# Kernel optimization log

Measured on AMD Instinct MI355X. Metric: run time of the kernel, lower is better.

## Reference

```python
import jax, jax.numpy as jnp
import numpy as np

B, S, D, H = 4, 1024, 1024, 16
HD = D // H


def setup_inputs() -> dict:
    key = jax.random.key(0)
    ks = jax.random.split(key, 12)
    s = 1.0 / np.sqrt(D)
    inp = {
        'q': jax.random.normal(ks[0], (B, S, D), jnp.float32),
        'k': jax.random.normal(ks[1], (B, S, D), jnp.float32),
        'v': jax.random.normal(ks[2], (B, S, D), jnp.float32),
        'mask': jnp.broadcast_to(jnp.tril(jnp.ones((S, S), jnp.int32)), (B, S, S)),
        'Wq': jax.random.uniform(ks[3], (D, D), jnp.float32, -s, s),
        'bq': jax.random.uniform(ks[4], (D,), jnp.float32, -s, s),
        'Wk': jax.random.uniform(ks[5], (D, D), jnp.float32, -s, s),
        'bk': jax.random.uniform(ks[6], (D,), jnp.float32, -s, s),
        'Wv': jax.random.uniform(ks[7], (D, D), jnp.float32, -s, s),
        'bv': jax.random.uniform(ks[8], (D,), jnp.float32, -s, s),
        'Wo': jax.random.uniform(ks[9], (D, D), jnp.float32, -s, s),
        'bo': jax.random.uniform(ks[10], (D,), jnp.float32, -s, s),
    }
    return inp


def _split_heads(x):
    # [B,S,D] -> [B,H,S,HD]
    b, s, d = x.shape
    return x.reshape(b, s, H, HD).transpose(0, 2, 1, 3)


def reference(q, k, v, mask, Wq, bq, Wk, bk, Wv, bv, Wo, bo):
    # Linear projections (torch Linear: x @ W.T + b) followed by relu
    qh = jax.nn.relu(q @ Wq.T + bq)
    kh = jax.nn.relu(k @ Wk.T + bk)
    vh = jax.nn.relu(v @ Wv.T + bv)
    qh, kh, vh = _split_heads(qh), _split_heads(kh), _split_heads(vh)
    scores = jnp.einsum('bhqd,bhkd->bhqk', qh, kh) / jnp.sqrt(jnp.float32(HD))
    scores = jnp.where(mask[:, None, :, :] == 0, jnp.float32(-1e9), scores)
    attn = jax.nn.softmax(scores, axis=-1)
    y = jnp.einsum('bhqk,bhkd->bhqd', attn, vh)
    y = y.transpose(0, 2, 1, 3).reshape(B, S, D)  # merge heads
    return jax.nn.relu(y @ Wo.T + bo)
```

## Files before the change

kernel.cpp:

```cpp
#include <hip/hip_runtime.h>


using f16    = _Float16;
using f16x4  = __attribute__((ext_vector_type(4))) _Float16;
using f16x8  = __attribute__((ext_vector_type(8))) _Float16;
using f32x4  = __attribute__((ext_vector_type(4))) float;
using f32x16 = __attribute__((ext_vector_type(16))) float;

static constexpr int S = 1024, Dm = 1024, NH = 16, HD = 64;

#if __has_builtin(__builtin_amdgcn_mfma_f32_32x32x16_f16)
#define USE_G32 1
#define MFMA32(ACC, A_, B_) \
    (ACC) = __builtin_amdgcn_mfma_f32_32x32x16_f16((A_), (B_), (ACC), 0, 0, 0)
#else
#define USE_G32 0
#endif

#if __has_builtin(__builtin_amdgcn_mfma_f32_16x16x32_f16) && \
    __has_builtin(__builtin_amdgcn_mfma_f32_16x16x16f16)
#define USE_A16 1
#define MFMA16K32(ACC, A_, B_) \
    (ACC) = __builtin_amdgcn_mfma_f32_16x16x32_f16((A_), (B_), (ACC), 0, 0, 0)
#define MFMA16(ACC, A_, B_) \
    (ACC) = __builtin_amdgcn_mfma_f32_16x16x16f16((A_), (B_), (ACC), 0, 0, 0)
#else
#define USE_A16 0
#endif

#define LO4(v) __builtin_shufflevector((v), (v), 0, 1, 2, 3)
#define HI4(v) __builtin_shufflevector((v), (v), 4, 5, 6, 7)

__device__ __forceinline__ f16x4 cvt4(float4 a) {
    f16x4 r; r[0] = (f16)a.x; r[1] = (f16)a.y; r[2] = (f16)a.z; r[3] = (f16)a.w;
    return r;
}

__device__ __forceinline__ int pcol64(int k) {
#if USE_A16
    return ((k >> 3) & 3) * 16 + ((k >> 5) << 3) + (k & 7);
#else
    return ((k >> 2) & 3) * 16 + ((k >> 4) << 2) + (k & 3);
#endif
}

__device__ __forceinline__ int swz(int row, int col) {
    return (col & ~31) | ((((col >> 3) ^ (row >> 1)) & 3) << 3) | (col & 7);
}

__device__ __forceinline__ void store_out(void* out, int mode, int m, int n, float v) {
    const int b_ = m >> 10, s_ = m & 1023, h_ = n >> 6, hd_ = n & 63;
    const size_t idx = (mode == 0)
        ? (((size_t)(b_ * NH + h_) * S + s_) * HD + pcol64(hd_))
        : (((size_t)(b_ * NH + h_) * HD + hd_) * S + s_);
    ((f16*)out)[idx] = (f16)v;
}

#if __has_builtin(__builtin_amdgcn_global_load_lds)
#define HAS_GLL 1
#else
#define HAS_GLL 0
#endif

__device__ __forceinline__ void gll16(const void* g, void* l) {
#if HAS_GLL
    __builtin_amdgcn_global_load_lds(
        (const __attribute__((address_space(1))) void*)g,
        (__attribute__((address_space(3))) void*)l, 16, 0, 0);
#else
    *(uint4*)l = *(const uint4*)g;
#endif
}

__global__ __launch_bounds__(256)
void cvt_w(const float* __restrict__ s0, const float* __restrict__ s1,
           const float* __restrict__ s2, f16* __restrict__ dst)
{
    const int z = blockIdx.y;
    const float* src = (z == 0) ? s0 : (z == 1) ? s1 : s2;
    const int e = blockIdx.x * 256 + threadIdx.x;
    const int n = e >> 8;
    const int k = (e & 255) * 4;
    const float4 v = *(const float4*)(src + (size_t)n * Dm + k);
    *(f16x4*)(dst + (size_t)z * Dm * Dm + (size_t)n * Dm + swz(n, k)) = cvt4(v);
}

__global__ __launch_bounds__(512, 6)
void gemm_qkv(const float* __restrict__ q, const float* __restrict__ k,
              const float* __restrict__ v, const f16* __restrict__ wqkv,
              const float* __restrict__ bq, const float* __restrict__ bk,
              const float* __restrict__ bv,
              f16* __restrict__ qh, f16* __restrict__ kh, f16* __restrict__ vt)
{
    const int z = blockIdx.z;
    const float* A = (z == 0) ? q : (z == 1) ? k : v;
    const float* bias = (z == 0) ? bq : (z == 1) ? bk : bv;
    f16* out = (z == 0) ? qh : (z == 1) ? kh : vt;
    const int mode = (z == 2) ? 1 : 0;
    const f16* Wf = wqkv + (size_t)z * Dm * Dm;

    const int tid = threadIdx.x;
    const int bm = blockIdx.x, bn = blockIdx.y;
#if USE_G32
    __shared__ alignas(16) float As[2][128][32];
    __shared__ alignas(16) f16   Ws[2][128][32];

    const int lane = tid & 63, wave = tid >> 6;
    const int l31 = lane & 31, kh2 = lane >> 5;
    const int wm = wave & 3, wn = wave >> 2;

    const int arow = tid >> 3;
    const int aslotD = tid & 7;
    const int aslotS = aslotD ^ (arow & 7);
    const float* Asrc0 = A + (size_t)(bm * 128 + arow) * Dm + aslotS * 4;
    const int wrow = tid >> 2, wcol = (tid & 3) * 8;
    const f16* Wsrc0 = Wf + (size_t)(bn * 128 + wrow) * Dm + wcol;

    auto dma = [&](int k0, int buf) {
        gll16(Asrc0 + k0,                      &As[buf][arow][aslotD * 4]);
        gll16(Asrc0 + (size_t)64 * Dm + k0,    &As[buf][64 + arow][aslotD * 4]);
        gll16(Wsrc0 + k0,                      &Ws[buf][wrow][wcol]);
    };

    auto afrag = [&](int buf, int r, int s) -> f16x8 {
        const int p = s * 4 + kh2 * 2, r7 = r & 7;
        const f32x4 lo = *(const f32x4*)&As[buf][r][(p ^ r7) * 4];
        const f32x4 hi = *(const f32x4*)&As[buf][r][((p + 1) ^ r7) * 4];
        f16x8 f;
        f[0] = (f16)lo[0]; f[1] = (f16)lo[1]; f[2] = (f16)lo[2]; f[3] = (f16)lo[3];
        f[4] = (f16)hi[0]; f[5] = (f16)hi[1]; f[6] = (f16)hi[2]; f[7] = (f16)hi[3];
        return f;
    };
    auto wfrag = [&](int buf, int r, int s) -> f16x8 {
        const int sl = s * 2 + kh2;
        return *(const f16x8*)&Ws[buf][r][((sl ^ (r >> 1)) & 3) * 8];
    };

    f32x16 acc[2] = {};
    auto kslice = [&](int buf, int s) {
        const f16x8 af  = afrag(buf, wm * 32 + l31, s);
        const f16x8 bf0 = wfrag(buf, wn * 64 + l31, s);
        const f16x8 bf1 = wfrag(buf, wn * 64 + 32 + l31, s);
        MFMA32(acc[0], af, bf0);
        MFMA32(acc[1], af, bf1);
    };

    constexpr int NIT = Dm / 32;
    dma(0, 0);
    for (int t = 0; t < NIT; ++t) {
        const int cur = t & 1;
        __syncthreads();
        if (t + 1 < NIT) dma((t + 1) * 32, cur ^ 1);
        kslice(cur, 0);
        kslice(cur, 1);
    }

#pragma unroll
    for (int j = 0; j < 2; ++j) {
        const int col = bn * 128 + wn * 64 + j * 32 + l31;
        const float bb = bias[col];
#pragma unroll
        for (int blk = 0; blk < 4; ++blk) {
            const int row0 = bm * 128 + wm * 32 + 8 * blk + 4 * kh2;
            if (mode == 1) {
                const int b_ = row0 >> 10, s_ = row0 & 1023;
                const int h_ = col >> 6, hd_ = col & 63;
                f16x4 vv;
#pragma unroll
                for (int r = 0; r < 4; ++r)
                    vv[r] = (f16)fmaxf(acc[j][blk * 4 + r] + bb, 0.0f);
                *(f16x4*)&out[((size_t)(b_ * NH + h_) * HD + hd_) * S + s_] = vv;
            } else {
#pragma unroll
                for (int r = 0; r < 4; ++r)
                    store_out(out, mode, row0 + r, col,
                              fmaxf(acc[j][blk * 4 + r] + bb, 0.0f));
            }
        }
    }
#else
    for (int i = tid; i < 128 * 128; i += 512) {
        const int m = bm * 128 + (i >> 7);
        const int n = bn * 128 + (i & 127);
        float acc = 0.0f;
        for (int k2 = 0; k2 < Dm; ++k2)
            acc = fmaf(A[(size_t)m * Dm + k2], (float)Wf[(size_t)n * Dm + swz(n, k2)], acc);
        store_out(out, mode, m, n, fmaxf(acc + bias[n], 0.0f));
    }
#endif
}

__global__ __launch_bounds__(256, 6)
void gemm_out(const f16* __restrict__ y, const float* __restrict__ wo,
              const float* __restrict__ bo, float* __restrict__ out)
{
    const int tid = threadIdx.x;
    const int bm = blockIdx.x, bn = blockIdx.y;
#if USE_G32
    __shared__ alignas(16) f16   As[2][64][32];
    __shared__ alignas(16) float Wsf[2][64][32];

    const int lane = tid & 63, wave = tid >> 6;
    const int l31 = lane & 31, kh2 = lane >> 5;
    const int wm = wave & 1, wn = wave >> 1;

    const int drow = tid >> 2, dcol = (tid & 3) * 8;
    const f16* Asrc = y + (size_t)(bm * 64 + drow) * Dm + dcol;
    const int wrow = tid >> 3;
    const int wslotD = tid & 7;
    const int wslotS = wslotD ^ (wrow & 7);
    const float* Wsrc0 = wo + (size_t)(bn * 64 + wrow) * Dm + wslotS * 4;

    auto dma = [&](int k0, int buf) {
        gll16(Asrc + k0, &As[buf][drow][dcol]);
        gll16(Wsrc0 + k0,                   &Wsf[buf][wrow][wslotD * 4]);
        gll16(Wsrc0 + (size_t)32 * Dm + k0, &Wsf[buf][32 + wrow][wslotD * 4]);
    };
    auto yfrag = [&](int buf, int r, int s) -> f16x8 {
        const int sl = s * 2 + kh2;
        return *(const f16x8*)&As[buf][r][((sl ^ (r >> 1)) & 3) * 8];
    };
    auto wfrag32 = [&](int buf, int r, int s) -> f16x8 {
        const int p = s * 4 + kh2 * 2, r7 = r & 7;
        const f32x4 lo = *(const f32x4*)&Wsf[buf][r][(p ^ r7) * 4];
        const f32x4 hi = *(const f32x4*)&Wsf[buf][r][((p + 1) ^ r7) * 4];
        f16x8 f;
        f[0] = (f16)lo[0]; f[1] = (f16)lo[1]; f[2] = (f16)lo[2]; f[3] = (f16)lo[3];
        f[4] = (f16)hi[0]; f[5] = (f16)hi[1]; f[6] = (f16)hi[2]; f[7] = (f16)hi[3];
        return f;
    };

    f32x16 acc = {};
    constexpr int NIT = Dm / 32;
    dma(0, 0);
    for (int t = 0; t < NIT; ++t) {
        const int cur = t & 1;
        __syncthreads();
        if (t + 1 < NIT) dma((t + 1) * 32, cur ^ 1);
#pragma unroll
        for (int s = 0; s < 2; ++s) {
            const f16x8 af = yfrag(cur, wm * 32 + l31, s);
            const f16x8 bf = wfrag32(cur, wn * 32 + l31, s);
            MFMA32(acc, af, bf);
        }
    }

    const int col = bn * 64 + wn * 32 + l31;
    const float bb = bo[col];
#pragma unroll
    for (int blk = 0; blk < 4; ++blk) {
        const int row0 = bm * 64 + wm * 32 + 8 * blk + 4 * kh2;
#pragma unroll
        for (int r = 0; r < 4; ++r)
            out[(size_t)(row0 + r) * Dm + col] = fmaxf(acc[blk * 4 + r] + bb, 0.0f);
    }
#else
    for (int i = tid; i < 64 * 64; i += 256) {
        const int m = bm * 64 + (i >> 6);
        const int n = bn * 64 + (i & 63);
        float acc = 0.0f;
        for (int k2 = 0; k2 < Dm; ++k2)
            acc = fmaf((float)y[(size_t)m * Dm + swz(m, k2)],
                       wo[(size_t)n * Dm + k2], acc);
        out[(size_t)m * Dm + n] = fmaxf(acc + bo[n], 0.0f);
    }
#endif
}

__global__ __launch_bounds__(512, 6)
void attn_fwd(const f16* __restrict__ qh, const f16* __restrict__ kh,
              const f16* __restrict__ vt, f16* __restrict__ y)
{
    const int bz = blockIdx.x;
    const int qt = bz & 7;
    const int h  = (bz >> 3) & 15;
    const int b  = bz >> 7;
    const size_t head = (size_t)(b * NH + h) * S * HD;

#if USE_A16
    __shared__ alignas(16) f16 Ks[2][64][72];
    __shared__ alignas(16) f16 Vs[2][64][72];

    const int tid  = threadIdx.x;
    const int wave = tid >> 6;
    const int lane = tid & 63;
    const int l15  = lane & 15;
    const int quad = lane >> 4;
    const int sr   = tid >> 3;
    const int t8   = tid & 7;

    const f16* Qrow = qh + head + (size_t)(qt * 128 + wave * 16 + l15) * HD;
    const f16* Kp   = kh + head;
    const f16* Vp   = vt + head;

    f16x8 aq[2];
    {
        const uint4 q0 = *(const uint4*)(Qrow + quad * 16);
        const uint4 q1 = *(const uint4*)(Qrow + quad * 16 + 8);
        aq[0] = *(f16x8*)&q0;
        aq[1] = *(f16x8*)&q1;
    }

    const int qg = qt * 128 + wave * 16 + l15;
    float m_i = -1e30f, l_i = 0.0f;
    f32x4 acc_o[4] = {};

    const int vc0 = 16 * ((2 * t8) & 3) + 4 * (t8 >> 1);
    const int vc1 = 16 * ((2 * t8 + 1) & 3) + 4 * (t8 >> 1);

    uint4 pk, pv;
    auto pref = [&](int kt) {
        pk = *(const uint4*)(Kp + (size_t)(kt * 64 + sr) * HD + t8 * 8);
        pv = *(const uint4*)(Vp + (size_t)sr * S + kt * 64 + t8 * 8);
    };

    const int ktmax = 2 * qt + 1;
    pref(0);
    for (int kt = 0; kt <= ktmax; ++kt) {
        const int cur = kt & 1;
        *(uint4*)&Ks[cur][sr][t8 * 8] = pk;
        {
            f16x8 pv8 = *(f16x8*)&pv;
            *(f16x4*)&Vs[cur][sr][vc0] = LO4(pv8);
            *(f16x4*)&Vs[cur][sr][vc1] = HI4(pv8);
        }
        __syncthreads();
        if (kt < ktmax) pref(kt + 1);

        f32x4 accs[4] = {};
#pragma unroll
        for (int t = 0; t < 4; ++t) {
            const f16x8 k8a = *(const f16x8*)&Ks[cur][t * 16 + l15][quad * 16];
            const f16x8 k8b = *(const f16x8*)&Ks[cur][t * 16 + l15][quad * 16 + 8];
            MFMA16K32(accs[t], k8a, aq[0]);
            MFMA16K32(accs[t], k8b, aq[1]);
        }

        const int key0 = kt * 64 + quad * 4;
#pragma unroll
        for (int t = 0; t < 4; ++t)
#pragma unroll
            for (int r = 0; r < 4; ++r) {
                float sv = accs[t][r] * 0.125f;
                if (key0 + t * 16 + r > qg) sv = -1e9f;
                accs[t][r] = sv;
            }

        float mx = accs[0][0];
#pragma unroll
        for (int t = 0; t < 4; ++t)
#pragma unroll
            for (int r = 0; r < 4; ++r) mx = fmaxf(mx, accs[t][r]);
        mx = fmaxf(mx, __shfl_xor(mx, 16, 64));
        mx = fmaxf(mx, __shfl_xor(mx, 32, 64));
        const float mnew = fmaxf(m_i, mx);
        float sm = 0.0f;
#pragma unroll
        for (int t = 0; t < 4; ++t)
#pragma unroll
            for (int r = 0; r < 4; ++r) {
                const float e = __expf(accs[t][r] - mnew);
                accs[t][r] = e;
                sm += e;
            }
        sm += __shfl_xor(sm, 16, 64);
        sm += __shfl_xor(sm, 32, 64);
        const float alpha = __expf(m_i - mnew);
        l_i = l_i * alpha + sm;
        m_i = mnew;

        f16x4 ap[4];
#pragma unroll
        for (int c = 0; c < 4; ++c) {
            f16x4 v;
#pragma unroll
            for (int j = 0; j < 4; ++j) v[j] = (f16)accs[c][j];
            ap[c] = v;
        }

        float ar[4];
#pragma unroll
        for (int r = 0; r < 4; ++r) ar[r] = __shfl(alpha, quad * 4 + r, 64);
#pragma unroll
        for (int t2 = 0; t2 < 4; ++t2)
#pragma unroll
            for (int r = 0; r < 4; ++r) acc_o[t2][r] *= ar[r];
#pragma unroll
        for (int t2 = 0; t2 < 4; ++t2) {
            const f16x8 v8a = *(const f16x8*)&Vs[cur][t2 * 16 + l15][quad * 16];
            const f16x8 v8b = *(const f16x8*)&Vs[cur][t2 * 16 + l15][quad * 16 + 8];
            MFMA16(acc_o[t2], ap[0], LO4(v8a));
            MFMA16(acc_o[t2], ap[1], HI4(v8a));
            MFMA16(acc_o[t2], ap[2], LO4(v8b));
            MFMA16(acc_o[t2], ap[3], HI4(v8b));
        }
    }

    float lr[4];
#pragma unroll
    for (int r = 0; r < 4; ++r) lr[r] = __shfl(l_i, quad * 4 + r, 64);
#pragma unroll
    for (int t2 = 0; t2 < 4; ++t2)
#pragma unroll
        for (int r = 0; r < 4; ++r) {
            const int srow = qt * 128 + wave * 16 + quad * 4 + r;
            const int dcol = h * 64 + t2 * 16 + l15;
            y[((size_t)b * S + srow) * Dm + swz(srow, dcol)] =
                (f16)(acc_o[t2][r] / lr[r]);
        }
#else
    const int tid = threadIdx.x;
    if (tid < 128) {
        const int q = qt * 128 + tid;
        const f16* Qr = qh + head + (size_t)q * HD;
        float qv[64];
        for (int d = 0; d < 64; ++d) qv[d] = (float)Qr[pcol64(d)];
        float mx = -1e30f;
        for (int key = 0; key <= q; ++key) {
            const f16* Kr = kh + head + (size_t)key * HD;
            float s = 0.0f;
            for (int d = 0; d < 64; ++d) s = fmaf(qv[d], (float)Kr[pcol64(d)], s);
            mx = fmaxf(mx, s * 0.125f);
        }
        float o[64];
        for (int d = 0; d < 64; ++d) o[d] = 0.0f;
        float l = 0.0f;
        for (int key = 0; key <= q; ++key) {
            const f16* Kr = kh + head + (size_t)key * HD;
            float s = 0.0f;
            for (int d = 0; d < 64; ++d) s = fmaf(qv[d], (float)Kr[pcol64(d)], s);
            const float p = __expf(s * 0.125f - mx);
            l += p;
            for (int d = 0; d < 64; ++d)
                o[d] = fmaf(p, (float)vt[head + (size_t)d * S + key], o[d]);
        }
        for (int d = 0; d < 64; ++d)
            y[((size_t)b * S + q) * Dm + swz(q, h * 64 + d)] = (f16)(o[d] / l);
    }
#endif
}

extern "C" void kernel_launch(void* const* d_in, const int* in_sizes, int n_in,
                              void* d_out, int out_size, void* d_ws, size_t ws_size,
                              hipStream_t stream)
{
    f16* ws = (f16*)d_ws;
    const size_t SEG = (size_t)4 * 1024 * 1024;
    f16* qh   = ws;
    f16* kh   = ws + SEG;
    f16* vt   = ws + 2 * SEG;
    f16* wqkv = ws + 3 * SEG;
    f16* y    = ws + 3 * SEG;

    cvt_w<<<dim3(1024, 3), 256, 0, stream>>>(
        (const float*)d_in[4], (const float*)d_in[6], (const float*)d_in[8], wqkv);
    gemm_qkv<<<dim3(32, 8, 3), 512, 0, stream>>>(
        (const float*)d_in[0], (const float*)d_in[1], (const float*)d_in[2],
        wqkv,
        (const float*)d_in[5], (const float*)d_in[7], (const float*)d_in[9],
        qh, kh, vt);
    attn_fwd<<<dim3(4 * NH * (S / 128)), 512, 0, stream>>>(qh, kh, vt, y);
    gemm_out<<<dim3(64, 16), 256, 0, stream>>>(
        y, (const float*)d_in[10], (const float*)d_in[11], (float*)d_out);
}
```

Measured before the change: 238.7 us.

## Rewrite attention with 32x32x16 MFMA, 4 waves of 32 query rows

The attention kernel moves from 16x16 MFMA tiles with 8 waves of 16 query rows to 32x32x16 MFMA tiles with 4 waves of 32 query rows each, launched with 256 threads. Q/K head layout drops the pcol64 column permutation, and the P operand is rebuilt through cross-half lane shuffles. Waves whose rows lie entirely above a key tile now skip that tile. The aim is fewer MFMA issues, fewer LDS reads per FLOP and less wasted causal work, at the cost of more registers per wave and fewer waves per block.

```diff
diff --git a/kernel.cpp b/kernel.cpp
--- a/kernel.cpp
+++ b/kernel.cpp
@@ -17,17 +17,6 @@
 #define USE_G32 0
 #endif
 
-#if __has_builtin(__builtin_amdgcn_mfma_f32_16x16x32_f16) && \
-    __has_builtin(__builtin_amdgcn_mfma_f32_16x16x16f16)
-#define USE_A16 1
-#define MFMA16K32(ACC, A_, B_) \
-    (ACC) = __builtin_amdgcn_mfma_f32_16x16x32_f16((A_), (B_), (ACC), 0, 0, 0)
-#define MFMA16(ACC, A_, B_) \
-    (ACC) = __builtin_amdgcn_mfma_f32_16x16x16f16((A_), (B_), (ACC), 0, 0, 0)
-#else
-#define USE_A16 0
-#endif
-
 #define LO4(v) __builtin_shufflevector((v), (v), 0, 1, 2, 3)
 #define HI4(v) __builtin_shufflevector((v), (v), 4, 5, 6, 7)
 
@@ -36,14 +25,6 @@
     return r;
 }
 
-__device__ __forceinline__ int pcol64(int k) {
-#if USE_A16
-    return ((k >> 3) & 3) * 16 + ((k >> 5) << 3) + (k & 7);
-#else
-    return ((k >> 2) & 3) * 16 + ((k >> 4) << 2) + (k & 3);
-#endif
-}
-
 __device__ __forceinline__ int swz(int row, int col) {
     return (col & ~31) | ((((col >> 3) ^ (row >> 1)) & 3) << 3) | (col & 7);
 }
@@ -51,7 +32,7 @@
 __device__ __forceinline__ void store_out(void* out, int mode, int m, int n, float v) {
     const int b_ = m >> 10, s_ = m & 1023, h_ = n >> 6, hd_ = n & 63;
     const size_t idx = (mode == 0)
-        ? (((size_t)(b_ * NH + h_) * S + s_) * HD + pcol64(hd_))
+        ? (((size_t)(b_ * NH + h_) * S + s_) * HD + hd_)
         : (((size_t)(b_ * NH + h_) * HD + hd_) * S + s_);
     ((f16*)out)[idx] = (f16)v;
 }
@@ -267,7 +248,7 @@
 #endif
 }
 
-__global__ __launch_bounds__(512, 6)
+__global__ __launch_bounds__(256, 4)
 void attn_fwd(const f16* __restrict__ qh, const f16* __restrict__ kh,
               const f16* __restrict__ vt, f16* __restrict__ y)
 {
@@ -277,149 +258,152 @@
     const int b  = bz >> 7;
     const size_t head = (size_t)(b * NH + h) * S * HD;
 
-#if USE_A16
+#if USE_G32
     __shared__ alignas(16) f16 Ks[2][64][72];
     __shared__ alignas(16) f16 Vs[2][64][72];
 
     const int tid  = threadIdx.x;
     const int wave = tid >> 6;
     const int lane = tid & 63;
-    const int l15  = lane & 15;
-    const int quad = lane >> 4;
-    const int sr   = tid >> 3;
-    const int t8   = tid & 7;
-
-    const f16* Qrow = qh + head + (size_t)(qt * 128 + wave * 16 + l15) * HD;
-    const f16* Kp   = kh + head;
-    const f16* Vp   = vt + head;
-
-    f16x8 aq[2];
-    {
-        const uint4 q0 = *(const uint4*)(Qrow + quad * 16);
-        const uint4 q1 = *(const uint4*)(Qrow + quad * 16 + 8);
-        aq[0] = *(f16x8*)&q0;
-        aq[1] = *(f16x8*)&q1;
-    }
-
-    const int qg = qt * 128 + wave * 16 + l15;
+    const int l31  = lane & 31;
+    const int kh2  = lane >> 5;
+    const int sr   = tid >> 2;
+    const int sc   = (tid & 3) * 16;
+
+    const int qrow = qt * 128 + wave * 32 + l31;
+    const f16* Qr = qh + head + (size_t)qrow * HD;
+    const f16* Kp = kh + head;
+    const f16* Vp = vt + head;
+
+    f16x8 aq[4];
+#pragma unroll
+    for (int s = 0; s < 4; ++s)
+        aq[s] = *(const f16x8*)(Qr + s * 16 + kh2 * 8);
+
     float m_i = -1e30f, l_i = 0.0f;
-    f32x4 acc_o[4] = {};
-
-    const int vc0 = 16 * ((2 * t8) & 3) + 4 * (t8 >> 1);
-    const int vc1 = 16 * ((2 * t8 + 1) & 3) + 4 * (t8 >> 1);
-
-    uint4 pk, pv;
+    f32x16 acc_o[2] = {};
+
+    uint4 pk[2], pv[2];
     auto pref = [&](int kt) {
-        pk = *(const uint4*)(Kp + (size_t)(kt * 64 + sr) * HD + t8 * 8);
-        pv = *(const uint4*)(Vp + (size_t)sr * S + kt * 64 + t8 * 8);
+        const f16* Krow = Kp + (size_t)(kt * 64 + sr) * HD + sc;
+        pk[0] = *(const uint4*)Krow;
+        pk[1] = *(const uint4*)(Krow + 8);
+        const f16* Vrow = Vp + (size_t)sr * S + kt * 64 + sc;
+        pv[0] = *(const uint4*)Vrow;
+        pv[1] = *(const uint4*)(Vrow + 8);
     };
 
     const int ktmax = 2 * qt + 1;
     pref(0);
     for (int kt = 0; kt <= ktmax; ++kt) {
         const int cur = kt & 1;
-        *(uint4*)&Ks[cur][sr][t8 * 8] = pk;
-        {
-            f16x8 pv8 = *(f16x8*)&pv;
-            *(f16x4*)&Vs[cur][sr][vc0] = LO4(pv8);
-            *(f16x4*)&Vs[cur][sr][vc1] = HI4(pv8);
-        }
+        *(uint4*)&Ks[cur][sr][sc]     = pk[0];
+        *(uint4*)&Ks[cur][sr][sc + 8] = pk[1];
+        *(uint4*)&Vs[cur][sr][sc]     = pv[0];
+        *(uint4*)&Vs[cur][sr][sc + 8] = pv[1];
         __syncthreads();
         if (kt < ktmax) pref(kt + 1);
 
-        f32x4 accs[4] = {};
-#pragma unroll
-        for (int t = 0; t < 4; ++t) {
-            const f16x8 k8a = *(const f16x8*)&Ks[cur][t * 16 + l15][quad * 16];
-            const f16x8 k8b = *(const f16x8*)&Ks[cur][t * 16 + l15][quad * 16 + 8];
-            MFMA16K32(accs[t], k8a, aq[0]);
-            MFMA16K32(accs[t], k8b, aq[1]);
-        }
-
-        const int key0 = kt * 64 + quad * 4;
-#pragma unroll
-        for (int t = 0; t < 4; ++t)
-#pragma unroll
-            for (int r = 0; r < 4; ++r) {
-                float sv = accs[t][r] * 0.125f;
-                if (key0 + t * 16 + r > qg) sv = -1e9f;
-                accs[t][r] = sv;
+        if (kt * 64 <= qt * 128 + wave * 32 + 31) {
+            f32x16 accs[2] = {};
+#pragma unroll
+            for (int g = 0; g < 2; ++g)
+#pragma unroll
+                for (int s = 0; s < 4; ++s) {
+                    const f16x8 kf =
+                        *(const f16x8*)&Ks[cur][g * 32 + l31][s * 16 + kh2 * 8];
+                    MFMA32(accs[g], kf, aq[s]);
+                }
+
+            const int key_base = kt * 64 + 4 * kh2;
+#pragma unroll
+            for (int g = 0; g < 2; ++g)
+#pragma unroll
+                for (int i = 0; i < 16; ++i) {
+                    const int key = key_base + g * 32 + 8 * (i >> 2) + (i & 3);
+                    float sv = accs[g][i] * 0.125f;
+                    if (key > qrow) sv = -1e9f;
+                    accs[g][i] = sv;
+                }
+
+            float mx = accs[0][0];
+#pragma unroll
+            for (int g = 0; g < 2; ++g)
+#pragma unroll
+                for (int i = 0; i < 16; ++i) mx = fmaxf(mx, accs[g][i]);
+            mx = fmaxf(mx, __shfl_xor(mx, 32, 64));
+            const float mnew = fmaxf(m_i, mx);
+            float sm = 0.0f;
+#pragma unroll
+            for (int g = 0; g < 2; ++g)
+#pragma unroll
+                for (int i = 0; i < 16; ++i) {
+                    const float e = __expf(accs[g][i] - mnew);
+                    accs[g][i] = e;
+                    sm += e;
+                }
+            sm += __shfl_xor(sm, 32, 64);
+            const float alpha = __expf(m_i - mnew);
+            l_i = l_i * alpha + sm;
+            m_i = mnew;
+
+#pragma unroll
+            for (int i = 0; i < 16; ++i) {
+                const float ar = __shfl(alpha, 8 * (i >> 2) + 4 * kh2 + (i & 3), 64);
+                acc_o[0][i] *= ar;
+                acc_o[1][i] *= ar;
             }
 
-        float mx = accs[0][0];
-#pragma unroll
-        for (int t = 0; t < 4; ++t)
-#pragma unroll
-            for (int r = 0; r < 4; ++r) mx = fmaxf(mx, accs[t][r]);
-        mx = fmaxf(mx, __shfl_xor(mx, 16, 64));
-        mx = fmaxf(mx, __shfl_xor(mx, 32, 64));
-        const float mnew = fmaxf(m_i, mx);
-        float sm = 0.0f;
-#pragma unroll
-        for (int t = 0; t < 4; ++t)
-#pragma unroll
-            for (int r = 0; r < 4; ++r) {
-                const float e = __expf(accs[t][r] - mnew);
-                accs[t][r] = e;
-                sm += e;
+#pragma unroll
+            for (int s = 0; s < 4; ++s) {
+                const int g = s >> 1;
+                const int bOwn  = ((s & 1) << 1) | kh2;
+                const int bGive = ((s & 1) << 1) | (kh2 ^ 1);
+                f16x4 own, giv;
+#pragma unroll
+                for (int r = 0; r < 4; ++r) {
+                    own[r] = (f16)accs[g][4 * bOwn + r];
+                    giv[r] = (f16)accs[g][4 * bGive + r];
+                }
+                uint2 gu = *(uint2*)&giv;
+                gu.x = __shfl_xor(gu.x, 32, 64);
+                gu.y = __shfl_xor(gu.y, 32, 64);
+                const f16x4 rcv = *(f16x4*)&gu;
+                const f16x8 ap = (kh2 == 0)
+                    ? __builtin_shufflevector(own, rcv, 0, 1, 2, 3, 4, 5, 6, 7)
+                    : __builtin_shufflevector(rcv, own, 0, 1, 2, 3, 4, 5, 6, 7);
+                const f16x8 v0 = *(const f16x8*)&Vs[cur][l31][s * 16 + kh2 * 8];
+                const f16x8 v1 = *(const f16x8*)&Vs[cur][32 + l31][s * 16 + kh2 * 8];
+                MFMA32(acc_o[0], ap, v0);
+                MFMA32(acc_o[1], ap, v1);
             }
-        sm += __shfl_xor(sm, 16, 64);
-        sm += __shfl_xor(sm, 32, 64);
-        const float alpha = __expf(m_i - mnew);
-        l_i = l_i * alpha + sm;
-        m_i = mnew;
-
-        f16x4 ap[4];
-#pragma unroll
-        for (int c = 0; c < 4; ++c) {
-            f16x4 v;
-#pragma unroll
-            for (int j = 0; j < 4; ++j) v[j] = (f16)accs[c][j];
-            ap[c] = v;
-        }
-
-        float ar[4];
-#pragma unroll
-        for (int r = 0; r < 4; ++r) ar[r] = __shfl(alpha, quad * 4 + r, 64);
-#pragma unroll
-        for (int t2 = 0; t2 < 4; ++t2)
-#pragma unroll
-            for (int r = 0; r < 4; ++r) acc_o[t2][r] *= ar[r];
-#pragma unroll
-        for (int t2 = 0; t2 < 4; ++t2) {
-            const f16x8 v8a = *(const f16x8*)&Vs[cur][t2 * 16 + l15][quad * 16];
-            const f16x8 v8b = *(const f16x8*)&Vs[cur][t2 * 16 + l15][quad * 16 + 8];
-            MFMA16(acc_o[t2], ap[0], LO4(v8a));
-            MFMA16(acc_o[t2], ap[1], HI4(v8a));
-            MFMA16(acc_o[t2], ap[2], LO4(v8b));
-            MFMA16(acc_o[t2], ap[3], HI4(v8b));
-        }
-    }
-
-    float lr[4];
-#pragma unroll
-    for (int r = 0; r < 4; ++r) lr[r] = __shfl(l_i, quad * 4 + r, 64);
-#pragma unroll
-    for (int t2 = 0; t2 < 4; ++t2)
-#pragma unroll
-        for (int r = 0; r < 4; ++r) {
-            const int srow = qt * 128 + wave * 16 + quad * 4 + r;
-            const int dcol = h * 64 + t2 * 16 + l15;
+        }
+    }
+
+#pragma unroll
+    for (int i = 0; i < 16; ++i) {
+        const int rl = 8 * (i >> 2) + 4 * kh2 + (i & 3);
+        const float li = __shfl(l_i, rl, 64);
+        const int srow = qt * 128 + wave * 32 + rl;
+#pragma unroll
+        for (int n = 0; n < 2; ++n) {
+            const int dcol = h * 64 + n * 32 + l31;
             y[((size_t)b * S + srow) * Dm + swz(srow, dcol)] =
-                (f16)(acc_o[t2][r] / lr[r]);
-        }
+                (f16)(acc_o[n][i] / li);
+        }
+    }
 #else
     const int tid = threadIdx.x;
     if (tid < 128) {
         const int q = qt * 128 + tid;
         const f16* Qr = qh + head + (size_t)q * HD;
         float qv[64];
-        for (int d = 0; d < 64; ++d) qv[d] = (float)Qr[pcol64(d)];
+        for (int d = 0; d < 64; ++d) qv[d] = (float)Qr[d];
         float mx = -1e30f;
         for (int key = 0; key <= q; ++key) {
             const f16* Kr = kh + head + (size_t)key * HD;
             float s = 0.0f;
-            for (int d = 0; d < 64; ++d) s = fmaf(qv[d], (float)Kr[pcol64(d)], s);
+            for (int d = 0; d < 64; ++d) s = fmaf(qv[d], (float)Kr[d], s);
             mx = fmaxf(mx, s * 0.125f);
         }
         float o[64];
@@ -428,7 +412,7 @@
         for (int key = 0; key <= q; ++key) {
             const f16* Kr = kh + head + (size_t)key * HD;
             float s = 0.0f;
-            for (int d = 0; d < 64; ++d) s = fmaf(qv[d], (float)Kr[pcol64(d)], s);
+            for (int d = 0; d < 64; ++d) s = fmaf(qv[d], (float)Kr[d], s);
             const float p = __expf(s * 0.125f - mx);
             l += p;
             for (int d = 0; d < 64; ++d)
@@ -459,7 +443,7 @@
         wqkv,
         (const float*)d_in[5], (const float*)d_in[7], (const float*)d_in[9],
         qh, kh, vt);
-    attn_fwd<<<dim3(4 * NH * (S / 128)), 512, 0, stream>>>(qh, kh, vt, y);
+    attn_fwd<<<dim3(4 * NH * (S / 128)), 256, 0, stream>>>(qh, kh, vt, y);
     gemm_out<<<dim3(64, 16), 256, 0, stream>>>(
         y, (const float*)d_in[10], (const float*)d_in[11], (float*)d_out);
 }
```

Result: slower. 362.7 us (+51.9%).
